# Kernel optimization log

Measured on AMD Instinct MI355X. Metric: run time of the kernel, lower is better.

The kernel has to match this reference:

```python
import jax, jax.numpy as jnp
import numpy as np

N, C, S, S2, H, CTX = 4, 512, 2048, 2048, 8, 512
EPS = 1e-5  # torch GroupNorm default


def setup_inputs() -> dict:
    key = jax.random.key(0)
    ks = jax.random.split(key, 6)
    sd = lambda fan: 1.0 / np.sqrt(fan)
    return {
        "input": jax.random.normal(ks[0], (N, C, S), jnp.float32),
        "context": jax.random.normal(ks[1], (N, CTX, S2), jnp.float32),
        "gamma": jnp.ones((C,), jnp.float32),
        "beta": jnp.zeros((C,), jnp.float32),
        "Wq": jax.random.normal(ks[2], (C * H, C), jnp.float32) * sd(C),
        "bq": jnp.zeros((C * H,), jnp.float32),
        "Wkv": jax.random.normal(ks[3], (C * H * 2, CTX), jnp.float32) * sd(CTX),
        "bkv": jnp.zeros((C * H * 2,), jnp.float32),
        "Wo": jax.random.normal(ks[4], (C, C * H), jnp.float32) * sd(C * H),
        "bo": jnp.zeros((C,), jnp.float32),
    }


def reference(input, context, gamma, beta, Wq, bq, Wkv, bkv, Wo, bo):
    n, c, s = input.shape
    h = H
    # GroupNorm(1, c): normalize over (C, S) per sample, per-channel affine
    mu = jnp.mean(input, axis=(1, 2), keepdims=True)
    var = jnp.var(input, axis=(1, 2), keepdims=True)
    xn = (input - mu) * jax.lax.rsqrt(var + EPS)
    xn = xn * gamma[None, :, None] + beta[None, :, None]
    # 1x1 conv projections == matmul over channel dim
    q = jnp.einsum('oc,ncs->nos', Wq, xn) + bq[None, :, None]          # [n, h*c, s]
    kv = jnp.einsum('od,nds->nos', Wkv, context) + bkv[None, :, None]  # [n, 2*h*c, s2]
    q = q.reshape(n, h, c, s).transpose(0, 1, 3, 2)                    # [n, h, s, c]
    kv = kv.reshape(n, 2 * h, c, -1).transpose(0, 1, 3, 2)             # [n, 2h, s2, c]
    k, v = kv[:, :h], kv[:, h:]
    scale = c ** (-0.25)
    att = jax.nn.softmax(
        jnp.einsum('nhqc,nhkc->nhqk', q * scale, k * scale), axis=-1)
    y = jnp.einsum('nhqk,nhkc->nhqc', att, v)                          # [n, h, s, c]
    y = y.transpose(0, 1, 3, 2).reshape(n, h * c, s)                   # b (h n) d
    out = jnp.einsum('co,nos->ncs', Wo, y) + bo[None, :, None]
    return input + out
```

## Files before the change

### kernel.cpp

```cpp
#include <hip/hip_runtime.h>
#include <cstdint>
#include <cstddef>


#define NB 4
#define CC 512
#define SS 2048
#define HH 8
#define QK_SCALE 0.044194173824159216f

typedef float  floatx4 __attribute__((ext_vector_type(4)));
typedef __bf16 bf16x8  __attribute__((ext_vector_type(8)));
typedef __bf16 bf16x4  __attribute__((ext_vector_type(4)));

__device__ __forceinline__ void async16(const void* g, void* l) {
  __builtin_amdgcn_global_load_lds((const __attribute__((address_space(1))) void*)g,
                                   (__attribute__((address_space(3))) void*)l, 16, 0, 0);
}

template <int N>
__device__ __forceinline__ float dpp_ror_f(float v) {
  return __builtin_bit_cast(
      float, __builtin_amdgcn_update_dpp(0, __builtin_bit_cast(int, v), 0x120 + N, 0xf, 0xf, true));
}
__device__ __forceinline__ float red_max16(float v) {
  v = fmaxf(v, dpp_ror_f<8>(v));
  v = fmaxf(v, dpp_ror_f<4>(v));
  v = fmaxf(v, dpp_ror_f<2>(v));
  v = fmaxf(v, dpp_ror_f<1>(v));
  return v;
}
__device__ __forceinline__ float red_sum16(float v) {
  v += dpp_ror_f<8>(v);
  v += dpp_ror_f<4>(v);
  v += dpp_ror_f<2>(v);
  v += dpp_ror_f<1>(v);
  return v;
}

__global__ void prep1(const float* __restrict__ x, float* __restrict__ part,
                      const float* __restrict__ Wq, __bf16* __restrict__ WqB,
                      const float* __restrict__ Wkv, __bf16* __restrict__ WkvB,
                      const float* __restrict__ Wo, __bf16* __restrict__ WoB) {
  const int bx = blockIdx.x;
  if (bx < 512) {
    const int n = bx >> 7, cidx = bx & 127;
    const float* p = x + (size_t)n * (CC * SS) + (size_t)cidx * 8192;
    float s = 0.f, q = 0.f;
    for (int j = 0; j < 8; ++j) {
      floatx4 v = *(const floatx4*)&p[(j * 256 + threadIdx.x) * 4];
      for (int e = 0; e < 4; ++e) { s += v[e]; q += v[e] * v[e]; }
    }
    for (int off = 32; off >= 1; off >>= 1) {
      s += __shfl_down(s, off, 64);
      q += __shfl_down(q, off, 64);
    }
    __shared__ float shS[4], shQ[4];
    const int wave = threadIdx.x >> 6, lane = threadIdx.x & 63;
    if (lane == 0) { shS[wave] = s; shQ[wave] = q; }
    __syncthreads();
    if (threadIdx.x == 0) {
      part[bx * 2] = shS[0] + shS[1] + shS[2] + shS[3];
      part[bx * 2 + 1] = shQ[0] + shQ[1] + shQ[2] + shQ[3];
    }
  } else {
    const int r = bx - 512;
    const int y = r >> 12, xb = r & 4095;
    const float* s = y == 0 ? Wq : (y == 1 ? Wkv : Wo);
    __bf16* d = y == 0 ? WqB : (y == 1 ? WkvB : WoB);
    const int cnt = y == 1 ? 1048576 : 524288;
    int idx = xb * 256 + threadIdx.x;
    if (idx >= cnt) return;
    floatx4 v = ((const floatx4*)s)[idx];
    bf16x4 pk;
    for (int e = 0; e < 4; ++e) pk[e] = (__bf16)v[e];
    ((bf16x4*)d)[idx] = pk;
  }
}

__global__ void ln_final(const float* __restrict__ part, float* __restrict__ muA,
                         float* __restrict__ rsA) {
  const int n = blockIdx.x, tid = threadIdx.x;
  float s = part[(n * 128 + tid) * 2];
  float q = part[(n * 128 + tid) * 2 + 1];
  for (int off = 32; off >= 1; off >>= 1) {
    s += __shfl_down(s, off, 64);
    q += __shfl_down(q, off, 64);
  }
  __shared__ float shS[2], shQ[2];
  const int wave = tid >> 6, lane = tid & 63;
  if (lane == 0) { shS[wave] = s; shQ[wave] = q; }
  __syncthreads();
  if (tid == 0) {
    float S = shS[0] + shS[1], Q = shQ[0] + shQ[1];
    const float inv = 1.f / (float)(CC * SS);
    float m = S * inv;
    float v = Q * inv - m * m;
    muA[n] = m;
    rsA[n] = rsqrtf(v + 1e-5f);
  }
}

__global__ void transpose_nc(const float* __restrict__ input, const float* __restrict__ context,
                             __bf16* __restrict__ xnT, __bf16* __restrict__ ctxT,
                             const float* __restrict__ mu, const float* __restrict__ rstd,
                             const float* __restrict__ gamma, const float* __restrict__ beta) {
  __shared__ float t[32][33];
  const int n = blockIdx.z >> 1, which = blockIdx.z & 1;
  const int c0 = blockIdx.y * 32, s0 = blockIdx.x * 32;
  const float* inp = (which ? context : input) + (size_t)n * CC * SS;
  __bf16* op = (which ? ctxT : xnT) + (size_t)n * SS * CC;
  const float muv = which ? 0.f : mu[n];
  const float rs = which ? 1.f : rstd[n];
  for (int i = 0; i < 4; ++i) {
    int c = c0 + threadIdx.y + i * 8;
    float x = inp[(size_t)c * SS + s0 + threadIdx.x];
    if (!which) x = (x - muv) * rs * gamma[c] + beta[c];
    t[threadIdx.y + i * 8][threadIdx.x] = x;
  }
  __syncthreads();
  for (int i = 0; i < 4; ++i) {
    int s = s0 + threadIdx.y + i * 8;
    op[(size_t)s * CC + c0 + threadIdx.x] = (__bf16)t[threadIdx.x][threadIdx.y + i * 8];
  }
}

__global__ void __launch_bounds__(512, 2) gemm_qkv(const __bf16* __restrict__ WqB,
                                                   const __bf16* __restrict__ WkvB,
                                                   const __bf16* __restrict__ xnT,
                                                   const __bf16* __restrict__ ctxT,
                                                   const float* __restrict__ bq,
                                                   const float* __restrict__ bkv,
                                                   __bf16* __restrict__ qT,
                                                   __bf16* __restrict__ kT,
                                                   __bf16* __restrict__ vv) {
  __shared__ __align__(16) char smem[256 * 264 * 2];
  __bf16* lA = (__bf16*)smem;
  __bf16* lB = (__bf16*)(smem + 65536);
  __bf16* lT = (__bf16*)smem;

  const int n = blockIdx.z, xb = blockIdx.x;
  const int n0 = blockIdx.y * 256;
  const bool isq = xb < 16;
  const int m0 = (isq ? xb : xb - 16) * 256;
  const __bf16* Aw = isq ? WqB : WkvB;
  const __bf16* Bt = (isq ? xnT : ctxT) + (size_t)n * SS * CC;
  const float* bias = isq ? bq : bkv;

  const int tid = threadIdx.x;
  const int wave = tid >> 6, lane = tid & 63;
  const int colv = lane & 15, g = lane >> 4;
  const int wr = wave >> 2, wc = wave & 3;
  const int lrow = lane >> 3, lch = lane & 7;

  auto stage = [&](int t, int buf) {
    const int k0 = t * 64;
    __bf16* dA = lA + buf * (256 * 64);
    __bf16* dB = lB + buf * (256 * 64);
#pragma unroll
    for (int j = 0; j < 4; ++j) {
      int r = wave * 32 + j * 8 + lrow;
      int ch = lch ^ (r & 7);
      async16(Aw + (size_t)(m0 + r) * 512 + k0 + ch * 8, dA + (wave * 32 + j * 8) * 64);
      async16(Bt + (size_t)(n0 + r) * 512 + k0 + ch * 8, dB + (wave * 32 + j * 8) * 64);
    }
  };

  floatx4 acc[8][4];
#pragma unroll
  for (int mf = 0; mf < 8; ++mf)
#pragma unroll
    for (int nf = 0; nf < 4; ++nf) acc[mf][nf] = (floatx4)0.f;

  stage(0, 0);
  stage(1, 1);
  asm volatile("s_waitcnt vmcnt(8)" ::: "memory");
  __builtin_amdgcn_s_barrier();

  for (int t = 0; t < 8; ++t) {
    const int buf = t & 1;
    const __bf16* cA = lA + buf * (256 * 64);
    const __bf16* cB = lB + buf * (256 * 64);
#pragma unroll
    for (int c = 0; c < 2; ++c) {
      bf16x8 bfr[4], af[4];
#pragma unroll
      for (int nf = 0; nf < 4; ++nf) {
        int rb = wc * 64 + nf * 16 + colv;
        bfr[nf] = *(const bf16x8*)&cB[rb * 64 + (((c * 4 + g) ^ (rb & 7)) << 3)];
      }
#pragma unroll
      for (int mf = 0; mf < 4; ++mf) {
        int ra = wr * 128 + mf * 16 + colv;
        af[mf] = *(const bf16x8*)&cA[ra * 64 + (((c * 4 + g) ^ (ra & 7)) << 3)];
      }
      __builtin_amdgcn_s_barrier();
      __builtin_amdgcn_s_setprio(1);
#pragma unroll
      for (int mf = 0; mf < 4; ++mf)
#pragma unroll
        for (int nf = 0; nf < 4; ++nf)
          acc[mf][nf] =
              __builtin_amdgcn_mfma_f32_16x16x32_bf16(af[mf], bfr[nf], acc[mf][nf], 0, 0, 0);
      __builtin_amdgcn_s_setprio(0);
      __builtin_amdgcn_s_barrier();
#pragma unroll
      for (int mf = 0; mf < 4; ++mf) {
        int ra = wr * 128 + 64 + mf * 16 + colv;
        af[mf] = *(const bf16x8*)&cA[ra * 64 + (((c * 4 + g) ^ (ra & 7)) << 3)];
      }
      __builtin_amdgcn_s_barrier();
      __builtin_amdgcn_s_setprio(1);
#pragma unroll
      for (int mf = 0; mf < 4; ++mf)
#pragma unroll
        for (int nf = 0; nf < 4; ++nf)
          acc[mf + 4][nf] =
              __builtin_amdgcn_mfma_f32_16x16x32_bf16(af[mf], bfr[nf], acc[mf + 4][nf], 0, 0, 0);
      __builtin_amdgcn_s_setprio(0);
      __builtin_amdgcn_s_barrier();
    }
    if (t < 6) {
      stage(t + 2, buf);
      asm volatile("s_waitcnt vmcnt(8)" ::: "memory");
    } else {
      asm volatile("s_waitcnt vmcnt(0)" ::: "memory");
    }
    __builtin_amdgcn_s_barrier();
  }

  if (isq || m0 < 4096) {
    __bf16* dst = (isq ? qT : kT) + (size_t)n * SS * 4096;
#pragma unroll
    for (int mf = 0; mf < 8; ++mf) {
      int mb = wr * 128 + mf * 16 + g * 4;
      floatx4 bv = *(const floatx4*)&bias[m0 + mb];
#pragma unroll
      for (int nf = 0; nf < 4; ++nf) {
        int nl = wc * 64 + nf * 16 + colv;
        bf16x4 pk;
#pragma unroll
        for (int i = 0; i < 4; ++i) pk[i] = (__bf16)(acc[mf][nf][i] + bv[i]);
        *(bf16x4*)&lT[nl * 264 + mb] = pk;
      }
    }
    asm volatile("s_waitcnt lgkmcnt(0)" ::: "memory");
    __builtin_amdgcn_s_barrier();
#pragma unroll
    for (int p = 0; p < 16; ++p) {
      int row = p * 16 + (tid >> 5);
      int ch = tid & 31;
      bf16x8 v = *(const bf16x8*)&lT[row * 264 + ch * 8];
      *(bf16x8*)&dst[(size_t)(n0 + row) * 4096 + m0 + ch * 8] = v;
    }
  } else {
    __bf16* vn = vv + (size_t)n * 4096 * SS;
#pragma unroll
    for (int mf = 0; mf < 8; ++mf) {
      int mb = wr * 128 + mf * 16 + g * 4;
      int o = m0 + mb - 4096;
      floatx4 bv = *(const floatx4*)&bias[m0 + mb];
#pragma unroll
      for (int nf = 0; nf < 4; ++nf) {
        int s = n0 + wc * 64 + nf * 16 + colv;
#pragma unroll
        for (int i = 0; i < 4; ++i)
          vn[(size_t)(o + i) * SS + s] = (__bf16)(acc[mf][nf][i] + bv[i]);
      }
    }
  }
}

__global__ void __launch_bounds__(256) flash_attn(const __bf16* __restrict__ qT,
                                                  const __bf16* __restrict__ kT,
                                                  const __bf16* __restrict__ vv,
                                                  __bf16* __restrict__ yT) {
  const int n = blockIdx.z, h = blockIdx.y, qt = blockIdx.x;
  const int tid = threadIdx.x;
  const int wave = tid >> 6, lane = tid & 63;
  const int colv = lane & 15, g = lane >> 4;

  const __bf16* qTn = qT + (size_t)n * SS * 4096;
  const __bf16* kTn = kT + (size_t)n * SS * 4096;
  const __bf16* vn  = vv + (size_t)n * 4096 * SS;
  __bf16* yTn = yT + (size_t)n * SS * 4096;

  const int qrow0 = qt * 64 + wave * 16;

  __shared__ __bf16 kbuf[32 * 512];
  __shared__ __bf16 vbuf[512 * 32];
  __shared__ __bf16 pbuf[4 * 16 * 88];
  __shared__ float axs[64];
  __shared__ float ils[64];

  bf16x8 qf[16];
  {
    const __bf16* qp = qTn + (size_t)(qrow0 + colv) * 4096 + h * 512 + g * 8;
#pragma unroll
    for (int kc = 0; kc < 16; ++kc) qf[kc] = *(const bf16x8*)(qp + kc * 32);
  }

  floatx4 Oacc[32];
#pragma unroll
  for (int t = 0; t < 32; ++t) Oacc[t] = (floatx4)0.f;
  float mrun[4] = {-1e30f, -1e30f, -1e30f, -1e30f};
  float lrun[4] = {0.f, 0.f, 0.f, 0.f};

  __bf16* pb = pbuf + wave * (16 * 88);

  auto stageK = [&](int kt) {
    const int key0 = kt * 32;
#pragma unroll
    for (int j = 0; j < 8; ++j) {
      int row = wave * 8 + j;
      const __bf16* src = kTn + (size_t)(key0 + row) * 4096 + h * 512 + ((lane ^ (row & 7)) << 3);
      async16(src, &kbuf[row * 512]);
    }
  };
  auto stageV = [&](int kt) {
    const int key0 = kt * 32;
#pragma unroll
    for (int j = 0; j < 8; ++j) {
      int i = wave * 8 + j;
      int row = i * 16 + (lane >> 2);
      int ch = (lane & 3) ^ (row & 3);
      const __bf16* src = vn + (size_t)(h * 512 + row) * SS + key0 + ch * 8;
      async16(src, &vbuf[i * 16 * 32]);
    }
  };

  stageK(0);
  stageV(0);

  for (int kt = 0; kt < 64; ++kt) {
    __syncthreads();

    floatx4 sc[2];
    sc[0] = (floatx4)0.f;
    sc[1] = (floatx4)0.f;
#pragma unroll
    for (int ct = 0; ct < 2; ++ct) {
      int key = ct * 16 + colv;
      const __bf16* kb = &kbuf[key * 512];
      int sw = key & 7;
#pragma unroll
      for (int kc = 0; kc < 16; ++kc) {
        bf16x8 bfr = *(const bf16x8*)(kb + (((kc * 4 + g) ^ sw) << 3));
        sc[ct] = __builtin_amdgcn_mfma_f32_16x16x32_bf16(qf[kc], bfr, sc[ct], 0, 0, 0);
      }
    }

    float p[2][4], alpha[4];
#pragma unroll
    for (int i = 0; i < 4; ++i) {
      float mx = red_max16(fmaxf(sc[0][i], sc[1][i]));
      float mnew = fmaxf(mrun[i], mx * QK_SCALE);
      alpha[i] = __expf(mrun[i] - mnew);
      float rs = 0.f;
#pragma unroll
      for (int ct = 0; ct < 2; ++ct) {
        float pvv = __expf(sc[ct][i] * QK_SCALE - mnew);
        p[ct][i] = pvv;
        rs += pvv;
      }
      rs = red_sum16(rs);
      lrun[i] = lrun[i] * alpha[i] + rs;
      mrun[i] = mnew;
    }
#pragma unroll
    for (int ct = 0; ct < 2; ++ct)
#pragma unroll
      for (int i = 0; i < 4; ++i)
        pb[(g * 4 + i) * 88 + ct * 16 + colv] = (__bf16)p[ct][i];
    if (colv == 0) {
      floatx4 av;
#pragma unroll
      for (int i = 0; i < 4; ++i) av[i] = alpha[i];
      *(floatx4*)&axs[wave * 16 + g * 4] = av;
    }
    __syncthreads();

    if (kt < 63) stageK(kt + 1);

#pragma unroll
    for (int qt4 = 0; qt4 < 4; ++qt4) {
      floatx4 av = *(const floatx4*)&axs[qt4 * 16 + g * 4];
#pragma unroll
      for (int dt = 0; dt < 8; ++dt) {
        floatx4 o = Oacc[qt4 * 8 + dt];
#pragma unroll
        for (int i = 0; i < 4; ++i) o[i] *= av[i];
        Oacc[qt4 * 8 + dt] = o;
      }
    }
    bf16x8 pa[4];
#pragma unroll
    for (int qt4 = 0; qt4 < 4; ++qt4)
      pa[qt4] = *(const bf16x8*)&pbuf[qt4 * (16 * 88) + colv * 88 + g * 8];
#pragma unroll
    for (int dt = 0; dt < 8; ++dt) {
      int drow = wave * 128 + dt * 16 + colv;
      bf16x8 vb = *(const bf16x8*)&vbuf[drow * 32 + ((g ^ (drow & 3)) << 3)];
#pragma unroll
      for (int qt4 = 0; qt4 < 4; ++qt4)
        Oacc[qt4 * 8 + dt] = __builtin_amdgcn_mfma_f32_16x16x32_bf16(pa[qt4], vb,
                                                                    Oacc[qt4 * 8 + dt], 0, 0, 0);
    }
    __syncthreads();
    if (kt < 63) stageV(kt + 1);
  }

  if (colv == 0) {
    floatx4 lv;
#pragma unroll
    for (int i = 0; i < 4; ++i) lv[i] = 1.f / lrun[i];
    *(floatx4*)&ils[wave * 16 + g * 4] = lv;
  }
  __syncthreads();
#pragma unroll
  for (int qt4 = 0; qt4 < 4; ++qt4) {
    floatx4 lv = *(const floatx4*)&ils[qt4 * 16 + g * 4];
#pragma unroll
    for (int dt = 0; dt < 8; ++dt)
#pragma unroll
      for (int i = 0; i < 4; ++i) {
        size_t idx = (size_t)(qt * 64 + qt4 * 16 + g * 4 + i) * 4096 + h * 512 + wave * 128 +
                     dt * 16 + colv;
        yTn[idx] = (__bf16)(Oacc[qt4 * 8 + dt][i] * lv[i]);
      }
  }
}

__global__ void __launch_bounds__(256) gemm_out_fused(const __bf16* __restrict__ Wo,
                                                      const __bf16* __restrict__ yT,
                                                      const float* __restrict__ bo,
                                                      const float* __restrict__ input,
                                                      float* __restrict__ out) {
  __shared__ __bf16 lA[128 * 64], lB[64 * 64];
  const int n = blockIdx.z;
  const int m0 = blockIdx.x * 128, n0 = blockIdx.y * 64;
  const __bf16* Bt = yT + (size_t)n * SS * 4096;
  const int tid = threadIdx.x;
  const int wave = tid >> 6, lane = tid & 63;
  const int colv = lane & 15, g = lane >> 4;
  const int lrow = lane >> 3, lch = lane & 7;

  floatx4 acc[2][4];
#pragma unroll
  for (int mt = 0; mt < 2; ++mt)
#pragma unroll
    for (int nt = 0; nt < 4; ++nt) acc[mt][nt] = (floatx4)0.f;

  for (int k0 = 0; k0 < 4096; k0 += 64) {
    __syncthreads();
#pragma unroll
    for (int j = 0; j < 4; ++j) {
      int r = wave * 32 + j * 8 + lrow;
      int ch = lch ^ (r & 7);
      async16(Wo + (size_t)(m0 + r) * 4096 + k0 + ch * 8, &lA[(wave * 32 + j * 8) * 64]);
    }
#pragma unroll
    for (int j = 0; j < 2; ++j) {
      int r = wave * 16 + j * 8 + lrow;
      int ch = lch ^ (r & 7);
      async16(Bt + (size_t)(n0 + r) * 4096 + k0 + ch * 8, &lB[(wave * 16 + j * 8) * 64]);
    }
    __syncthreads();
#pragma unroll
    for (int c = 0; c < 2; ++c) {
      bf16x8 af[2], bf[4];
#pragma unroll
      for (int t = 0; t < 2; ++t) {
        int r = wave * 32 + t * 16 + colv;
        af[t] = *(const bf16x8*)&lA[r * 64 + (((c * 4 + g) ^ (r & 7)) << 3)];
      }
#pragma unroll
      for (int t = 0; t < 4; ++t) {
        int rb = t * 16 + colv;
        bf[t] = *(const bf16x8*)&lB[rb * 64 + (((c * 4 + g) ^ (rb & 7)) << 3)];
      }
#pragma unroll
      for (int mt = 0; mt < 2; ++mt)
#pragma unroll
        for (int nt = 0; nt < 4; ++nt)
          acc[mt][nt] = __builtin_amdgcn_mfma_f32_16x16x32_bf16(af[mt], bf[nt], acc[mt][nt], 0, 0, 0);
    }
  }
#pragma unroll
  for (int mt = 0; mt < 2; ++mt) {
#pragma unroll
    for (int i = 0; i < 4; ++i) {
      int c = m0 + wave * 32 + mt * 16 + g * 4 + i;
      float bov = bo[c];
      size_t rowb = ((size_t)n * CC + c) * SS;
#pragma unroll
      for (int nt = 0; nt < 4; ++nt) {
        int s = n0 + nt * 16 + colv;
        out[rowb + s] = acc[mt][nt][i] + bov + input[rowb + s];
      }
    }
  }
}

extern "C" void kernel_launch(void* const* d_in, const int* in_sizes, int n_in,
                              void* d_out, int out_size, void* d_ws, size_t ws_size,
                              hipStream_t stream) {
  const float* input   = (const float*)d_in[0];
  const float* context = (const float*)d_in[1];
  const float* gamma   = (const float*)d_in[2];
  const float* beta    = (const float*)d_in[3];
  const float* Wq      = (const float*)d_in[4];
  const float* bq      = (const float*)d_in[5];
  const float* Wkv     = (const float*)d_in[6];
  const float* bkv     = (const float*)d_in[7];
  const float* Wo      = (const float*)d_in[8];
  const float* bo      = (const float*)d_in[9];
  float* out = (float*)d_out;
  (void)in_sizes; (void)n_in; (void)out_size;

  char* ws = (char*)d_ws;
  size_t off = 0;
  auto alloc = [&](size_t b) {
    void* p = ws + off;
    off = (off + b + 255) & ~(size_t)255;
    return p;
  };
  float*  lnp  = (float*)alloc((size_t)4 * 128 * 2 * sizeof(float));
  float*  muA  = (float*)alloc(4 * sizeof(float));
  float*  rsA  = (float*)alloc(4 * sizeof(float));
  __bf16* WqB  = (__bf16*)alloc((size_t)4096 * 512 * 2);
  __bf16* WkvB = (__bf16*)alloc((size_t)8192 * 512 * 2);
  __bf16* WoB  = (__bf16*)alloc((size_t)512 * 4096 * 2);
  __bf16* xnT  = (__bf16*)alloc((size_t)NB * SS * CC * 2);
  __bf16* ctxT = (__bf16*)alloc((size_t)NB * SS * CC * 2);

  const size_t PB = (size_t)SS * 4096 * 2;

  prep1<<<dim3(512 + 3 * 4096), dim3(256), 0, stream>>>(input, lnp, Wq, WqB, Wkv, WkvB, Wo, WoB);
  ln_final<<<dim3(4), dim3(128), 0, stream>>>(lnp, muA, rsA);
  transpose_nc<<<dim3(64, 16, 8), dim3(32, 8), 0, stream>>>(input, context, xnT, ctxT, muA, rsA,
                                                            gamma, beta);

  const size_t MiB = 1ull << 20;
  if (ws_size >= off + 16 * PB + 8 * MiB) {
    __bf16* qTb = (__bf16*)alloc(NB * PB);
    __bf16* kTb = (__bf16*)alloc(NB * PB);
    __bf16* vB  = (__bf16*)alloc(NB * PB);
    __bf16* yTb = (__bf16*)alloc(NB * PB);
    gemm_qkv<<<dim3(48, 8, 4), dim3(512), 0, stream>>>(WqB, WkvB, xnT, ctxT, bq, bkv, qTb, kTb,
                                                       vB);
    flash_attn<<<dim3(32, 8, 4), dim3(256), 0, stream>>>(qTb, kTb, vB, yTb);
    gemm_out_fused<<<dim3(4, 32, 4), dim3(256), 0, stream>>>(WoB, yTb, bo, input, out);
  } else if (ws_size >= off + 7 * PB + 8 * MiB) {
    __bf16* qTb = (__bf16*)alloc(PB);
    __bf16* kTb = (__bf16*)alloc(PB);
    __bf16* vB  = (__bf16*)alloc(PB);
    __bf16* yTb = (__bf16*)alloc(NB * PB);
    for (int n = 0; n < NB; ++n) {
      gemm_qkv<<<dim3(48, 8, 1), dim3(512), 0, stream>>>(WqB, WkvB, xnT + (size_t)n * SS * CC,
                                                         ctxT + (size_t)n * SS * CC, bq, bkv,
                                                         qTb, kTb, vB);
      flash_attn<<<dim3(32, 8, 1), dim3(256), 0, stream>>>(qTb, kTb, vB,
                                                           yTb + (size_t)n * SS * 4096);
    }
    gemm_out_fused<<<dim3(4, 32, 4), dim3(256), 0, stream>>>(WoB, yTb, bo, input, out);
  } else {
    __bf16* qTb = (__bf16*)alloc(PB);
    __bf16* kTb = (__bf16*)alloc(PB);
    __bf16* vB  = (__bf16*)alloc(PB);
    __bf16* yTb = (__bf16*)alloc(PB);
    for (int n = 0; n < NB; ++n) {
      gemm_qkv<<<dim3(48, 8, 1), dim3(512), 0, stream>>>(WqB, WkvB, xnT + (size_t)n * SS * CC,
                                                         ctxT + (size_t)n * SS * CC, bq, bkv,
                                                         qTb, kTb, vB);
      flash_attn<<<dim3(32, 8, 1), dim3(256), 0, stream>>>(qTb, kTb, vB, yTb);
      gemm_out_fused<<<dim3(4, 32, 1), dim3(256), 0, stream>>>(WoB, yTb, bo,
                                                               input + (size_t)n * CC * SS,
                                                               out + (size_t)n * CC * SS);
    }
  }
}
```

Baseline: 1.050 ms.

## Triple-buffer output GEMM with 128x128 tiles and 512-thread blocks

Rewrites the output projection GEMM to use 128x128 tiles with 8 waves in a 2x4 arrangement, and three LDS buffers filled by async global-to-LDS loads issued three K-steps ahead. Explicit vmcnt waits and barriers replace the per-step sync-load-sync pattern, so memory loads overlap with MFMA work and each loaded byte is reused more. In exchange it uses more LDS (96KB) and launches half as many blocks, which may lower occupancy. The hand-counted vmcnt values must match the number of loads each stage issues.

Result: no change. 1.060 ms (+0.9%).

```diff
diff --git a/kernel.cpp b/kernel.cpp
--- a/kernel.cpp
+++ b/kernel.cpp
@@ -431,71 +431,90 @@
   }
 }
 
-__global__ void __launch_bounds__(256) gemm_out_fused(const __bf16* __restrict__ Wo,
+__global__ void __launch_bounds__(512) gemm_out_fused(const __bf16* __restrict__ Wo,
                                                       const __bf16* __restrict__ yT,
                                                       const float* __restrict__ bo,
                                                       const float* __restrict__ input,
                                                       float* __restrict__ out) {
-  __shared__ __bf16 lA[128 * 64], lB[64 * 64];
+  __shared__ __bf16 lA[3][128 * 64], lB[3][128 * 64];
   const int n = blockIdx.z;
-  const int m0 = blockIdx.x * 128, n0 = blockIdx.y * 64;
+  const int m0 = blockIdx.x * 128, n0 = blockIdx.y * 128;
   const __bf16* Bt = yT + (size_t)n * SS * 4096;
   const int tid = threadIdx.x;
   const int wave = tid >> 6, lane = tid & 63;
   const int colv = lane & 15, g = lane >> 4;
+  const int wr = wave >> 2, wc = wave & 3;
   const int lrow = lane >> 3, lch = lane & 7;
 
-  floatx4 acc[2][4];
-#pragma unroll
-  for (int mt = 0; mt < 2; ++mt)
-#pragma unroll
-    for (int nt = 0; nt < 4; ++nt) acc[mt][nt] = (floatx4)0.f;
-
-  for (int k0 = 0; k0 < 4096; k0 += 64) {
-    __syncthreads();
-#pragma unroll
-    for (int j = 0; j < 4; ++j) {
-      int r = wave * 32 + j * 8 + lrow;
-      int ch = lch ^ (r & 7);
-      async16(Wo + (size_t)(m0 + r) * 4096 + k0 + ch * 8, &lA[(wave * 32 + j * 8) * 64]);
-    }
+  auto stage = [&](int t, int buf) {
+    const int k0 = t * 64;
 #pragma unroll
     for (int j = 0; j < 2; ++j) {
       int r = wave * 16 + j * 8 + lrow;
       int ch = lch ^ (r & 7);
-      async16(Bt + (size_t)(n0 + r) * 4096 + k0 + ch * 8, &lB[(wave * 16 + j * 8) * 64]);
-    }
-    __syncthreads();
+      async16(Wo + (size_t)(m0 + r) * 4096 + k0 + ch * 8, &lA[buf][(wave * 16 + j * 8) * 64]);
+      async16(Bt + (size_t)(n0 + r) * 4096 + k0 + ch * 8, &lB[buf][(wave * 16 + j * 8) * 64]);
+    }
+  };
+
+  floatx4 acc[4][2];
+#pragma unroll
+  for (int mt = 0; mt < 4; ++mt)
+#pragma unroll
+    for (int nt = 0; nt < 2; ++nt) acc[mt][nt] = (floatx4)0.f;
+
+  stage(0, 0);
+  stage(1, 1);
+  stage(2, 2);
+  asm volatile("s_waitcnt vmcnt(8)" ::: "memory");
+  __builtin_amdgcn_s_barrier();
+
+  int buf = 0;
+  for (int t = 0; t < 64; ++t) {
 #pragma unroll
     for (int c = 0; c < 2; ++c) {
-      bf16x8 af[2], bf[4];
-#pragma unroll
-      for (int t = 0; t < 2; ++t) {
-        int r = wave * 32 + t * 16 + colv;
-        af[t] = *(const bf16x8*)&lA[r * 64 + (((c * 4 + g) ^ (r & 7)) << 3)];
-      }
-#pragma unroll
-      for (int t = 0; t < 4; ++t) {
-        int rb = t * 16 + colv;
-        bf[t] = *(const bf16x8*)&lB[rb * 64 + (((c * 4 + g) ^ (rb & 7)) << 3)];
-      }
-#pragma unroll
-      for (int mt = 0; mt < 2; ++mt)
-#pragma unroll
-        for (int nt = 0; nt < 4; ++nt)
-          acc[mt][nt] = __builtin_amdgcn_mfma_f32_16x16x32_bf16(af[mt], bf[nt], acc[mt][nt], 0, 0, 0);
-    }
-  }
-#pragma unroll
-  for (int mt = 0; mt < 2; ++mt) {
+      bf16x8 af[4], bf[2];
+#pragma unroll
+      for (int mt = 0; mt < 4; ++mt) {
+        int ra = wr * 64 + mt * 16 + colv;
+        af[mt] = *(const bf16x8*)&lA[buf][ra * 64 + (((c * 4 + g) ^ (ra & 7)) << 3)];
+      }
+#pragma unroll
+      for (int nt = 0; nt < 2; ++nt) {
+        int rb = wc * 32 + nt * 16 + colv;
+        bf[nt] = *(const bf16x8*)&lB[buf][rb * 64 + (((c * 4 + g) ^ (rb & 7)) << 3)];
+      }
+#pragma unroll
+      for (int mt = 0; mt < 4; ++mt)
+#pragma unroll
+        for (int nt = 0; nt < 2; ++nt)
+          acc[mt][nt] =
+              __builtin_amdgcn_mfma_f32_16x16x32_bf16(af[mt], bf[nt], acc[mt][nt], 0, 0, 0);
+    }
+    if (t == 63) break;
+    __builtin_amdgcn_s_barrier();
+    if (t < 61) {
+      stage(t + 3, buf);
+      asm volatile("s_waitcnt vmcnt(8)" ::: "memory");
+    } else if (t == 61) {
+      asm volatile("s_waitcnt vmcnt(4)" ::: "memory");
+    } else {
+      asm volatile("s_waitcnt vmcnt(0)" ::: "memory");
+    }
+    __builtin_amdgcn_s_barrier();
+    buf = (buf == 2) ? 0 : buf + 1;
+  }
+
+#pragma unroll
+  for (int mt = 0; mt < 4; ++mt) {
 #pragma unroll
     for (int i = 0; i < 4; ++i) {
-      int c = m0 + wave * 32 + mt * 16 + g * 4 + i;
+      int c = m0 + wr * 64 + mt * 16 + g * 4 + i;
       float bov = bo[c];
       size_t rowb = ((size_t)n * CC + c) * SS;
 #pragma unroll
-      for (int nt = 0; nt < 4; ++nt) {
-        int s = n0 + nt * 16 + colv;
+      for (int nt = 0; nt < 2; ++nt) {
+        int s = n0 + wc * 32 + nt * 16 + colv;
         out[rowb + s] = acc[mt][nt][i] + bov + input[rowb + s];
       }
     }
@@ -550,7 +569,7 @@
     gemm_qkv<<<dim3(48, 8, 4), dim3(512), 0, stream>>>(WqB, WkvB, xnT, ctxT, bq, bkv, qTb, kTb,
                                                        vB);
     flash_attn<<<dim3(32, 8, 4), dim3(256), 0, stream>>>(qTb, kTb, vB, yTb);
-    gemm_out_fused<<<dim3(4, 32, 4), dim3(256), 0, stream>>>(WoB, yTb, bo, input, out);
+    gemm_out_fused<<<dim3(4, 16, 4), dim3(512), 0, stream>>>(WoB, yTb, bo, input, out);
   } else if (ws_size >= off + 7 * PB + 8 * MiB) {
     __bf16* qTb = (__bf16*)alloc(PB);
     __bf16* kTb = (__bf16*)alloc(PB);
@@ -563,7 +582,7 @@
       flash_attn<<<dim3(32, 8, 1), dim3(256), 0, stream>>>(qTb, kTb, vB,
                                                            yTb + (size_t)n * SS * 4096);
     }
-    gemm_out_fused<<<dim3(4, 32, 4), dim3(256), 0, stream>>>(WoB, yTb, bo, input, out);
+    gemm_out_fused<<<dim3(4, 16, 4), dim3(512), 0, stream>>>(WoB, yTb, bo, input, out);
   } else {
     __bf16* qTb = (__bf16*)alloc(PB);
     __bf16* kTb = (__bf16*)alloc(PB);
@@ -574,7 +593,7 @@
                                                          ctxT + (size_t)n * SS * CC, bq, bkv,
                                                          qTb, kTb, vB);
       flash_attn<<<dim3(32, 8, 1), dim3(256), 0, stream>>>(qTb, kTb, vB, yTb);
-      gemm_out_fused<<<dim3(4, 32, 1), dim3(256), 0, stream>>>(WoB, yTb, bo,
+      gemm_out_fused<<<dim3(4, 16, 1), dim3(512), 0, stream>>>(WoB, yTb, bo,
                                                                input + (size_t)n * CC * SS,
                                                                out + (size_t)n * CC * SS);
     }
```
